# Kernel optimization log

Hardware: AMD Instinct MI355X
Metric: run time of the kernel (lower is better)

Reference implementation:

```python
import jax, jax.numpy as jnp
import numpy as np

FILTER = 3
STRIDE = 1


def setup_inputs() -> dict:
    key = jax.random.key(0)
    ks = jax.random.split(key, 6)
    B, P, N, d_in, d_ein, d_model = 16, 4, 4096, 128, 32, 128
    e_dim = FILTER * (FILTER - 1) * d_ein  # 192
    adj = jax.random.uniform(ks[0], (N, N), jnp.float32)
    features = jax.random.normal(ks[1], (B, N, d_in), jnp.float32)
    edge_features = jax.random.normal(ks[2], (B, N, e_dim), jnp.float32)
    mask = jax.random.uniform(ks[3], (P, N, 1), jnp.float32)
    W = jax.random.normal(ks[4], (FILTER * d_in + e_dim, d_model), jnp.float32) * 0.02
    b = jnp.zeros((d_model,), jnp.float32)
    return dict(adj=adj, features=features, edge_features=edge_features, mask=mask, W=W, b=b)


def reference(adj, features, edge_features, mask, W, b):
    Fs, S = FILTER, STRIDE
    B, N, d_in = features.shape
    # padding rule from _padding(): below_pad = filter - (N % stride or stride)
    below_pad = N % S
    below_pad = S if below_pad == 0 else below_pad
    below_pad = Fs - below_pad  # = 2 for stride=1, filter=3
    n_out = (N + below_pad - Fs) // S + 1  # = N

    feat_pad = jnp.pad(features, ((0, 0), (0, below_pad), (0, 0)))
    idx = jnp.arange(n_out)[:, None] * S + jnp.arange(Fs)[None, :]  # [n_out, F]
    win = feat_pad[:, idx, :]  # [B, n_out, F, d_in] (gather = torch unfold windows)
    jump = win.mean(axis=2)    # features.unfold(...).sum(-1)/filter -> [B, n_out, d_in]
    # torch unfold puts filter dim last: [B, n_out, d_in, F]; flatten(-2,-1) is d_in-major
    feat_flat = jnp.swapaxes(win, -1, -2).reshape(B, n_out, Fs * d_in)

    mask_pad = jnp.pad(mask, ((0, 0), (0, below_pad), (0, 0)))
    m = mask_pad[:, idx, :].max(axis=2)  # [P, n_out, 1]

    feat_cat = jnp.concatenate([feat_flat, edge_features], axis=-1)  # [B, n_out, 576]
    out = jax.nn.relu(feat_cat @ W + b)  # dropout is identity in eval
    res = out + jump  # residual (res=True)

    P = m.shape[0]
    d_model = out.shape[-1]
    out_m = (m * out.reshape(-1, P, n_out, d_model)).reshape(-1, n_out, d_model)
    res_m = (m * res.reshape(-1, P, n_out, d_model)).reshape(-1, n_out, d_model)
    return adj, res_m, out_m, m
```

## Files before the change

kernel.cpp:

```cpp
#include <hip/hip_runtime.h>
#include <hip/hip_bf16.h>

typedef __attribute__((ext_vector_type(8))) short short8;
typedef __attribute__((ext_vector_type(4))) float floatx4;

#define NN     4096
#define DIN    128
#define EDIM   192
#define DMODEL 128

__device__ __forceinline__ unsigned short f2bf(float f) {
    union { float f; unsigned int i; } x; x.f = f;
    unsigned int u = x.i;
    u += 0x7FFFu + ((u >> 16) & 1u);
    return (unsigned short)(u >> 16);
}

__device__ __forceinline__ unsigned int pk2(float lo, float hi) {
    union { __hip_bfloat162 v; unsigned int u; } cv;
    cv.v = __float22bfloat162_rn(make_float2(lo, hi));
    return cv.u;
}

__device__ __forceinline__ short8 cvt8(const float4 a, const float4 b) {
    union { short8 s; unsigned int u[4]; } r;
    r.u[0] = pk2(a.x, a.y);
    r.u[1] = pk2(a.z, a.w);
    r.u[2] = pk2(b.x, b.y);
    r.u[3] = pk2(b.z, b.w);
    return r.s;
}

__global__ void prep_w(const float* __restrict__ W, unsigned short* __restrict__ wf) {
    const int t = blockIdx.x * 256 + threadIdx.x;
    const int jj   = t & 7;
    const int lane = (t >> 3) & 63;
    const int ct   = (t >> 9) & 7;
    const int gs   = t >> 12;
    const int kt = gs * 32 + ((lane >> 4) << 3) + jj;
    const int korig = (kt < 384) ? ((kt & 127) * 3 + (kt >> 7)) : kt;
    const int n = ct * 16 + (lane & 15);
    wf[t] = f2bf(W[korig * DMODEL + n]);
}

__global__ void prep_m(const float* __restrict__ mask,
                       float* __restrict__ m3f, float* __restrict__ o_m) {
    const int t = blockIdx.x * 256 + threadIdx.x;
    const int i = t & (NN - 1);
    float v = mask[t];
    if (i + 1 < NN) v = fmaxf(v, mask[t + 1]);
    if (i + 2 < NN) v = fmaxf(v, mask[t + 2]);
    m3f[t] = v;
    o_m[t] = v;
}

__global__ __launch_bounds__(256) void copy_adj(const float4* __restrict__ src,
                                                float4* __restrict__ dst) {
    int idx = blockIdx.x * 256 + threadIdx.x;
    #pragma unroll
    for (int i = 0; i < 16; ++i)
        dst[idx + i * 262144] = src[idx + i * 262144];
}

__global__ __launch_bounds__(256, 2) void main_k(
    const float* __restrict__ feat,
    const float* __restrict__ edgef,
    const unsigned short* __restrict__ wfrag,
    const float* __restrict__ bias,
    const float* __restrict__ m3f,
    float* __restrict__ o_res,
    float* __restrict__ o_out)
{
    const int tid  = threadIdx.x;
    const int lane = tid & 63;
    const int wv   = tid >> 6;
    const int nn   = lane & 15;
    const int quad = lane >> 4;

    const int blk = blockIdx.x;
    const int b   = blk >> 5;
    const int i0  = (blk & 31) << 7;

    const float* fb = feat  + (size_t)b * NN * DIN;
    const float* eb = edgef + (size_t)b * NN * EDIM;

    const int rowb = i0 + wv * 32 + nn;

    floatx4 acc[2][8];
    #pragma unroll
    for (int rt = 0; rt < 2; ++rt)
        #pragma unroll
        for (int ct = 0; ct < 8; ++ct)
            acc[rt][ct] = (floatx4){0.f, 0.f, 0.f, 0.f};

    const short8* wf8 = (const short8*)wfrag;

    #pragma unroll
    for (int j = 0; j < 3; ++j) {
        #pragma unroll
        for (int sl = 0; sl < 4; ++sl) {
            const int gs = j * 4 + sl;
            short8 bfr[8];
            #pragma unroll
            for (int ct = 0; ct < 8; ++ct)
                bfr[ct] = wf8[(gs * 8 + ct) * 64 + lane];
            short8 afr[2];
            #pragma unroll
            for (int rt = 0; rt < 2; ++rt) {
                const int row = rowb + rt * 16 + j;
                float4 a0 = make_float4(0.f, 0.f, 0.f, 0.f);
                float4 a1 = a0;
                if (row < NN) {
                    const float* s = fb + (size_t)row * DIN + sl * 32 + quad * 8;
                    a0 = *(const float4*)s;
                    a1 = *(const float4*)(s + 4);
                }
                afr[rt] = cvt8(a0, a1);
            }
            #pragma unroll
            for (int rt = 0; rt < 2; ++rt)
                #pragma unroll
                for (int ct = 0; ct < 8; ++ct)
                    acc[rt][ct] = __builtin_amdgcn_mfma_f32_16x16x32_bf16(
                        afr[rt], bfr[ct], acc[rt][ct], 0, 0, 0);
        }
    }

    #pragma unroll
    for (int eg = 0; eg < 6; ++eg) {
        const int gs = 12 + eg;
        short8 bfr[8];
        #pragma unroll
        for (int ct = 0; ct < 8; ++ct)
            bfr[ct] = wf8[(gs * 8 + ct) * 64 + lane];
        short8 afr[2];
        #pragma unroll
        for (int rt = 0; rt < 2; ++rt) {
            const int row = rowb + rt * 16;
            const float* s = eb + (size_t)row * EDIM + eg * 32 + quad * 8;
            const float4 a0 = *(const float4*)s;
            const float4 a1 = *(const float4*)(s + 4);
            afr[rt] = cvt8(a0, a1);
        }
        #pragma unroll
        for (int rt = 0; rt < 2; ++rt)
            #pragma unroll
            for (int ct = 0; ct < 8; ++ct)
                acc[rt][ct] = __builtin_amdgcn_mfma_f32_16x16x32_bf16(
                    afr[rt], bfr[ct], acc[rt][ct], 0, 0, 0);
    }

    float biasv[8];
    #pragma unroll
    for (int ct = 0; ct < 8; ++ct)
        biasv[ct] = bias[ct * 16 + nn];

    const int   p    = b & 3;
    const float inv3 = 1.0f / 3.0f;

    #pragma unroll
    for (int rt = 0; rt < 2; ++rt) {
        const int rbase = wv * 32 + rt * 16 + quad * 4;
        float mv[4];
        #pragma unroll
        for (int reg = 0; reg < 4; ++reg)
            mv[reg] = m3f[p * NN + i0 + rbase + reg];
        #pragma unroll
        for (int ct = 0; ct < 8; ++ct) {
            const int col = ct * 16 + nn;
            float fv[6];
            #pragma unroll
            for (int t6 = 0; t6 < 6; ++t6) {
                const int row = i0 + rbase + t6;
                fv[t6] = (row < NN) ? fb[(size_t)row * DIN + col] : 0.f;
            }
            #pragma unroll
            for (int reg = 0; reg < 4; ++reg) {
                float o = acc[rt][ct][reg] + biasv[ct];
                o = fmaxf(o, 0.f);
                const float jmp = (fv[reg] + fv[reg + 1] + fv[reg + 2]) * inv3;
                const size_t off = ((size_t)b * NN + (i0 + rbase + reg)) * DMODEL + col;
                const float mm = mv[reg];
                o_out[off] = mm * o;
                o_res[off] = mm * (o + jmp);
            }
        }
    }
}

extern "C" void kernel_launch(void* const* d_in, const int* in_sizes, int n_in,
                              void* d_out, int out_size, void* d_ws, size_t ws_size,
                              hipStream_t stream) {
    const float* adj   = (const float*)d_in[0];
    const float* feat  = (const float*)d_in[1];
    const float* edgef = (const float*)d_in[2];
    const float* mask  = (const float*)d_in[3];
    const float* W     = (const float*)d_in[4];
    const float* bias  = (const float*)d_in[5];

    float* out   = (float*)d_out;
    float* o_adj = out;
    float* o_res = out + (size_t)16777216;
    float* o_out = o_res + (size_t)8388608;
    float* o_m   = o_out + (size_t)8388608;

    unsigned short* wfrag = (unsigned short*)d_ws;
    float*          m3f   = (float*)((char*)d_ws + 73728 * 2);

    copy_adj<<<1024, 256, 0, stream>>>((const float4*)adj, (float4*)o_adj);
    prep_w<<<288, 256, 0, stream>>>(W, wfrag);
    prep_m<<<64, 256, 0, stream>>>(mask, m3f, o_m);
    main_k<<<512, 256, 0, stream>>>(feat, edgef, wfrag, bias, m3f, o_res, o_out);
}
```

Baseline: 284.0 us.

## Fuse adjacency copy and mask pooling into main kernel with nontemporal stores

Removes the separate adjacency-copy and mask-pooling kernels. Each main-kernel block now computes its 128-row window max of the mask into shared memory, writes the pooled mask output when b<4, and copies a slice of the adjacency matrix after its GEMM epilogue. Output and adjacency stores use nontemporal hints to avoid polluting caches. This cuts two launches and lets the copy overlap with compute in other blocks, at the cost of longer per-block tails and extra work in the occupancy-limited kernel.

```diff
diff --git a/kernel.cpp b/kernel.cpp
--- a/kernel.cpp
+++ b/kernel.cpp
@@ -43,34 +43,20 @@
     wf[t] = f2bf(W[korig * DMODEL + n]);
 }
 
-__global__ void prep_m(const float* __restrict__ mask,
-                       float* __restrict__ m3f, float* __restrict__ o_m) {
-    const int t = blockIdx.x * 256 + threadIdx.x;
-    const int i = t & (NN - 1);
-    float v = mask[t];
-    if (i + 1 < NN) v = fmaxf(v, mask[t + 1]);
-    if (i + 2 < NN) v = fmaxf(v, mask[t + 2]);
-    m3f[t] = v;
-    o_m[t] = v;
-}
-
-__global__ __launch_bounds__(256) void copy_adj(const float4* __restrict__ src,
-                                                float4* __restrict__ dst) {
-    int idx = blockIdx.x * 256 + threadIdx.x;
-    #pragma unroll
-    for (int i = 0; i < 16; ++i)
-        dst[idx + i * 262144] = src[idx + i * 262144];
-}
-
 __global__ __launch_bounds__(256, 2) void main_k(
     const float* __restrict__ feat,
     const float* __restrict__ edgef,
     const unsigned short* __restrict__ wfrag,
     const float* __restrict__ bias,
-    const float* __restrict__ m3f,
+    const float* __restrict__ mask,
+    const floatx4* __restrict__ adj4,
+    floatx4* __restrict__ o_adj4,
     float* __restrict__ o_res,
-    float* __restrict__ o_out)
+    float* __restrict__ o_out,
+    float* __restrict__ o_m)
 {
+    __shared__ float m3s[128];
+
     const int tid  = threadIdx.x;
     const int lane = tid & 63;
     const int wv   = tid >> 6;
@@ -80,6 +66,17 @@
     const int blk = blockIdx.x;
     const int b   = blk >> 5;
     const int i0  = (blk & 31) << 7;
+    const int p   = b & 3;
+
+    if (tid < 128) {
+        const int i = i0 + tid;
+        float v = mask[p * NN + i];
+        if (i + 1 < NN) v = fmaxf(v, mask[p * NN + i + 1]);
+        if (i + 2 < NN) v = fmaxf(v, mask[p * NN + i + 2]);
+        m3s[tid] = v;
+        if (b < 4) o_m[p * NN + i] = v;
+    }
+    __syncthreads();
 
     const float* fb = feat  + (size_t)b * NN * DIN;
     const float* eb = edgef + (size_t)b * NN * EDIM;
@@ -155,7 +152,6 @@
     for (int ct = 0; ct < 8; ++ct)
         biasv[ct] = bias[ct * 16 + nn];
 
-    const int   p    = b & 3;
     const float inv3 = 1.0f / 3.0f;
 
     #pragma unroll
@@ -164,7 +160,7 @@
         float mv[4];
         #pragma unroll
         for (int reg = 0; reg < 4; ++reg)
-            mv[reg] = m3f[p * NN + i0 + rbase + reg];
+            mv[reg] = m3s[rbase + reg];
         #pragma unroll
         for (int ct = 0; ct < 8; ++ct) {
             const int col = ct * 16 + nn;
@@ -181,9 +177,18 @@
                 const float jmp = (fv[reg] + fv[reg + 1] + fv[reg + 2]) * inv3;
                 const size_t off = ((size_t)b * NN + (i0 + rbase + reg)) * DMODEL + col;
                 const float mm = mv[reg];
-                o_out[off] = mm * o;
-                o_res[off] = mm * (o + jmp);
+                __builtin_nontemporal_store(mm * o, &o_out[off]);
+                __builtin_nontemporal_store(mm * (o + jmp), &o_res[off]);
             }
+        }
+    }
+
+    {
+        const int idx = blk * 256 + tid;
+        #pragma unroll
+        for (int i = 0; i < 32; ++i) {
+            const floatx4 v = __builtin_nontemporal_load(&adj4[idx + i * 131072]);
+            __builtin_nontemporal_store(v, &o_adj4[idx + i * 131072]);
         }
     }
 }
@@ -205,10 +210,9 @@
     float* o_m   = o_out + (size_t)8388608;
 
     unsigned short* wfrag = (unsigned short*)d_ws;
-    float*          m3f   = (float*)((char*)d_ws + 73728 * 2);
-
-    copy_adj<<<1024, 256, 0, stream>>>((const float4*)adj, (float4*)o_adj);
+
     prep_w<<<288, 256, 0, stream>>>(W, wfrag);
-    prep_m<<<64, 256, 0, stream>>>(mask, m3f, o_m);
-    main_k<<<512, 256, 0, stream>>>(feat, edgef, wfrag, bias, m3f, o_res, o_out);
-}
+    main_k<<<512, 256, 0, stream>>>(feat, edgef, wfrag, bias, mask,
+                                    (const floatx4*)adj, (floatx4*)o_adj,
+                                    o_res, o_out, o_m);
+}
```

Measured after the change: 273.7 us. 1.04x faster.
